# Kernel optimization log

Hardware: AMD Instinct MI355X
Metric: run time of the kernel (lower is better)

Reference implementation:

```python
import jax, jax.numpy as jnp
import numpy as np

V, J, NB = 6890, 52, 16
NPOSE = (J - 1) * 9  # 459 pose-blendshape features
# Standard SMPL-H kinematic tree: 22 body joints + left hand (wrist 20) + right hand (wrist 21)
PARENTS = np.array([
    -1, 0, 0, 0, 1, 2, 3, 4, 5, 6, 7, 8, 9, 9, 9, 12, 13, 14, 16, 17, 18, 19,
    20, 22, 23, 20, 25, 26, 20, 28, 29, 20, 31, 32, 20, 34, 35,
    21, 37, 38, 21, 40, 41, 21, 43, 44, 21, 46, 47, 21, 49, 50
], dtype=np.int32)


def rot6d_to_matrix(d6):
    # d6: (..., 6) -> (..., 3, 3), rows are the Gram-Schmidt basis (pytorch3d convention)
    a1, a2 = d6[..., :3], d6[..., 3:]
    b1 = a1 / jnp.linalg.norm(a1, axis=-1, keepdims=True)
    a2p = a2 - jnp.sum(b1 * a2, axis=-1, keepdims=True) * b1
    b2 = a2p / jnp.linalg.norm(a2p, axis=-1, keepdims=True)
    b3 = jnp.cross(b1, b2)
    return jnp.stack([b1, b2, b3], axis=-2)


def rigid_transform(rot_mats, joints):
    # rot_mats: (B, J, 3, 3); joints: (B, J, 3) -> relative transforms (B, J, 4, 4)
    rel = jnp.concatenate(
        [joints[..., :1, :], joints[..., 1:, :] - joints[..., PARENTS[1:], :]], axis=-2)
    tm = jnp.concatenate([rot_mats, rel[..., None]], axis=-1)  # (B, J, 3, 4)
    bottom = jnp.zeros(tm.shape[:-2] + (1, 4), dtype=tm.dtype).at[..., 0, 3].set(1.0)
    tm = jnp.concatenate([tm, bottom], axis=-2)  # (B, J, 4, 4)
    chain = [tm[..., 0, :, :]]
    for i in range(1, J):  # fixed 52-joint tree, unrolled
        chain.append(chain[int(PARENTS[i])] @ tm[..., i, :, :])
    transforms = jnp.stack(chain, axis=-3)  # (B, J, 4, 4)
    t_corr = jnp.einsum('bjcd,bjd->bjc', transforms[..., :3, :3], joints)
    return transforms.at[..., :3, 3].add(-t_corr)


def lbs_forward(body_pose, betas, global_orient, transl,
                v_template, shapedirs, posedirs, J_template, J_shapedirs, lbs_weights):
    full_pose = jnp.concatenate([global_orient, body_pose], axis=-2)  # (B, 52, 6)
    rot_mats = rot6d_to_matrix(full_pose)                              # (B, 52, 3, 3)
    joints = J_template + jnp.einsum('bk,jck->bjc', betas, J_shapedirs)
    A = rigid_transform(rot_mats, joints)                              # (B, 52, 4, 4)
    eye = jnp.eye(3, dtype=rot_mats.dtype)
    pose_feature = (rot_mats[..., 1:, :, :] - eye).reshape(rot_mats.shape[0], NPOSE)
    v_posed = (v_template
               + jnp.einsum('bk,vck->bvc', betas, shapedirs)
               + jnp.einsum('bk,kvc->bvc', pose_feature, posedirs))    # (B, V, 3)
    T = jnp.einsum('vj,bjcd->bvcd', lbs_weights, A)                    # (B, V, 4, 4)
    verts = jnp.einsum('bvcd,bvd->bvc', T[..., :3, :3], v_posed) + T[..., :3, 3]
    return verts + transl[..., None, :]


def setup_inputs() -> dict:
    key = jax.random.key(0)
    ks = jax.random.split(key, 10)
    B = 1024
    return {
        'body_pose': jax.random.normal(ks[0], (B, J - 1, 6), jnp.float32),
        'betas': jax.random.normal(ks[1], (B, NB), jnp.float32),
        'global_orient': jax.random.normal(ks[2], (B, 1, 6), jnp.float32),
        'transl': jax.random.normal(ks[3], (B, 3), jnp.float32),
        'v_template': jax.random.normal(ks[4], (V, 3), jnp.float32) * 0.3,
        'shapedirs': jax.random.normal(ks[5], (V, 3, NB), jnp.float32) * 0.01,
        'posedirs': jax.random.normal(ks[6], (NPOSE, V, 3), jnp.float32) * 0.01,
        'J_template': jax.random.normal(ks[7], (J, 3), jnp.float32) * 0.3,
        'J_shapedirs': jax.random.normal(ks[8], (J, 3, NB), jnp.float32) * 0.01,
        'lbs_weights': jax.nn.softmax(jax.random.normal(ks[9], (V, J), jnp.float32) * 2.0, axis=-1),
    }


def reference(body_pose, betas, global_orient, transl,
              v_template, shapedirs, posedirs, J_template, J_shapedirs, lbs_weights):
    return lbs_forward(body_pose, betas, global_orient, transl,
                       v_template, shapedirs, posedirs, J_template, J_shapedirs, lbs_weights)
```

## Files before the change

kernel.cpp:

```cpp
#include <hip/hip_runtime.h>

typedef unsigned short u16;
typedef __bf16  bf16x8 __attribute__((ext_vector_type(8)));
typedef float   f32x4  __attribute__((ext_vector_type(4)));
typedef unsigned int u32x4 __attribute__((ext_vector_type(4)));

#define B_SZ   1024
#define V_SZ   6890
#define VPADB  6912
#define J_SZ   52
#define NB_SZ  16
#define NPOSE  459
#define N3     20670
#define NPAD   20736
#define KG     480
#define KA     160
#define MROWS  12288

#define NK1    (B_SZ / 4)
#define NK0W   (VPADB / 64)
#define NK0    (648 * 15)

__constant__ int PARENTS_D[52] = {-1,0,0,0,1,2,3,4,5,6,7,8,9,9,9,12,13,14,16,17,18,19,20,22,23,
                                  20,25,26,20,28,29,20,31,32,20,34,35,21,37,38,21,40,41,21,43,44,
                                  21,46,47,21,49,50};

__device__ __forceinline__ u16 f2b(float f) {
  union { float f; unsigned u; } v; v.f = f;
  unsigned r = (v.u + 0x7FFFu + ((v.u >> 16) & 1u)) >> 16;
  return (u16)r;
}
__device__ __forceinline__ float b2f(u16 h) {
  union { unsigned u; float f; } v; v.u = ((unsigned)h) << 16;
  return v.f;
}
__device__ __forceinline__ void async16(const void* g, void* l) {
  __builtin_amdgcn_global_load_lds((const __attribute__((address_space(1))) void*)g,
                                   (__attribute__((address_space(3))) void*)l, 16, 0, 0);
}

__global__ __launch_bounds__(256) void k_prep(const float* __restrict__ posedirs,
                                              const float* __restrict__ shapedirs,
                                              const float* __restrict__ lbsw,
                                              const float* __restrict__ body_pose,
                                              const float* __restrict__ betas,
                                              const float* __restrict__ global_orient,
                                              const float* __restrict__ J_template,
                                              const float* __restrict__ J_shapedirs,
                                              u16* __restrict__ PDt,
                                              u16* __restrict__ WB,
                                              u16* __restrict__ AH,
                                              u16* __restrict__ PF)
{
  __shared__ __align__(16) char smem[35328];
  const int bid = blockIdx.x;
  const int tid = threadIdx.x;

  if (bid < NK1) {
    const int g = tid >> 6;
    const int t = tid & 63;
    const int b = bid * 4 + g;
    char* base = smem + g * 8832;
    float (*R)[9]   = (float(*)[9])(base);
    float (*jts)[3] = (float(*)[3])(base + 1872);
    float (*G)[12]  = (float(*)[12])(base + 2496);
    u16*   AHs      = (u16*)(base + 4992);

    for (int i = t; i < 12 * KA / 2; i += 64) ((unsigned*)AHs)[i] = 0u;

    if (t < J_SZ) {
      const float* d6 = (t == 0) ? &global_orient[(size_t)b * 6]
                                 : &body_pose[((size_t)b * 51 + (t - 1)) * 6];
      float a1x = d6[0], a1y = d6[1], a1z = d6[2];
      float a2x = d6[3], a2y = d6[4], a2z = d6[5];
      float inv1 = rsqrtf(a1x*a1x + a1y*a1y + a1z*a1z);
      float b1x = a1x*inv1, b1y = a1y*inv1, b1z = a1z*inv1;
      float d   = b1x*a2x + b1y*a2y + b1z*a2z;
      float ux = a2x - d*b1x, uy = a2y - d*b1y, uz = a2z - d*b1z;
      float inv2 = rsqrtf(ux*ux + uy*uy + uz*uz);
      float b2x = ux*inv2, b2y = uy*inv2, b2z = uz*inv2;
      float b3x = b1y*b2z - b1z*b2y;
      float b3y = b1z*b2x - b1x*b2z;
      float b3z = b1x*b2y - b1y*b2x;
      R[t][0]=b1x; R[t][1]=b1y; R[t][2]=b1z;
      R[t][3]=b2x; R[t][4]=b2y; R[t][5]=b2z;
      R[t][6]=b3x; R[t][7]=b3y; R[t][8]=b3z;
#pragma unroll
      for (int c = 0; c < 3; ++c) {
        float s = J_template[t*3 + c];
#pragma unroll
        for (int k = 0; k < NB_SZ; ++k)
          s += betas[(size_t)b*NB_SZ + k] * J_shapedirs[(t*3 + c)*NB_SZ + k];
        jts[t][c] = s;
      }
    }
    __syncthreads();

    if (t < 3) {
      const int c = t;
      G[0][c*4+0] = R[0][c*3+0];
      G[0][c*4+1] = R[0][c*3+1];
      G[0][c*4+2] = R[0][c*3+2];
      G[0][c*4+3] = jts[0][c];
      for (int j = 1; j < J_SZ; ++j) {
        int p = PARENTS_D[j];
        float r0 = jts[j][0] - jts[p][0];
        float r1 = jts[j][1] - jts[p][1];
        float r2 = jts[j][2] - jts[p][2];
        float g0 = G[p][c*4+0], g1 = G[p][c*4+1], g2 = G[p][c*4+2];
        G[j][c*4+0] = g0*R[j][0] + g1*R[j][3] + g2*R[j][6];
        G[j][c*4+1] = g0*R[j][1] + g1*R[j][4] + g2*R[j][7];
        G[j][c*4+2] = g0*R[j][2] + g1*R[j][5] + g2*R[j][8];
        G[j][c*4+3] = g0*r0 + g1*r1 + g2*r2 + G[p][c*4+3];
      }
    }
    __syncthreads();

    if (t < J_SZ) {
      float o[12];
#pragma unroll
      for (int i = 0; i < 12; ++i) o[i] = G[t][i];
#pragma unroll
      for (int c = 0; c < 3; ++c)
        o[c*4+3] -= o[c*4+0]*jts[t][0] + o[c*4+1]*jts[t][1] + o[c*4+2]*jts[t][2];
#pragma unroll
      for (int cd = 0; cd < 12; ++cd) {
        u16 hi = f2b(o[cd]);
        u16 lo = f2b(o[cd] - b2f(hi));
        AHs[cd*KA + t]        = hi;
        AHs[cd*KA + 52 + t]   = lo;
        AHs[cd*KA + 104 + t]  = hi;
      }
    }

    for (int k = t; k < KG; k += 64) {
      float val = 0.f;
      if (k < NPOSE) {
        int j  = k / 9 + 1;
        int rc = k - (j - 1) * 9;
        val = R[j][rc] - ((rc == 0 || rc == 4 || rc == 8) ? 1.f : 0.f);
      } else if (k < NPOSE + NB_SZ) {
        val = betas[(size_t)b*NB_SZ + (k - NPOSE)];
      }
      PF[(size_t)b*KG + k] = f2b(val);
    }

    __syncthreads();
    unsigned* dst = (unsigned*)(AH + (size_t)b * 12 * KA);
    for (int i = t; i < 12 * KA / 2; i += 64) dst[i] = ((const unsigned*)AHs)[i];

  } else if (bid < NK1 + NK0W) {
    u16* wtile = (u16*)smem;
    const int v0  = (bid - NK1) * 64;
    const int vl  = tid >> 2;
    const int v   = v0 + vl;
    const int jseg = (tid & 3) * 13;

    wtile[vl * KA + 156 + (tid & 3)] = 0;

#pragma unroll
    for (int jj = 0; jj < 13; ++jj) {
      int j = jseg + jj;
      float wv = (v < V_SZ) ? lbsw[(size_t)v * J_SZ + j] : 0.f;
      u16 hi = f2b(wv);
      u16 lo = f2b(wv - b2f(hi));
      wtile[vl * KA + j]        = hi;
      wtile[vl * KA + 52 + j]   = hi;
      wtile[vl * KA + 104 + j]  = lo;
    }
    __syncthreads();
    u32x4*       dst = (u32x4*)(WB + (size_t)v0 * KA);
    const u32x4* src = (const u32x4*)wtile;
    for (int i = tid; i < 64 * KA / 8; i += 256) dst[i] = src[i];

  } else {
    u16 (*tile)[33] = (u16(*)[33])smem;
    const int cb = bid - NK1 - NK0W;
    const int tx = tid & 31;
    const int ty = tid >> 5;
    const int n0 = (cb % 648) * 32;
    const int k0 = (cb / 648) * 32;
#pragma unroll
    for (int i = 0; i < 4; ++i) {
      int k = k0 + ty + i*8;
      int n = n0 + tx;
      float val = 0.f;
      if (n < N3) {
        if (k < NPOSE)              val = posedirs[(size_t)k * N3 + n];
        else if (k < NPOSE + NB_SZ) val = shapedirs[(size_t)n * NB_SZ + (k - NPOSE)];
      }
      tile[ty + i*8][tx] = f2b(val);
    }
    __syncthreads();
#pragma unroll
    for (int i = 0; i < 4; ++i) {
      int n = n0 + ty + i*8;
      int k = k0 + tx;
      int vv = n / 3;
      int cc = n - vv * 3;
      PDt[((size_t)cc * VPADB + vv) * KG + k] = tile[tx][ty + i*8];
    }
  }
}

__global__ __launch_bounds__(256) void k2_gemm(const u16* __restrict__ PF,
                                               const u16* __restrict__ PDt,
                                               const float* __restrict__ vtmpl,
                                               u16* __restrict__ VP)
{
  __shared__ __align__(16) u16 lA[2][4096];
  __shared__ __align__(16) u16 lB[2][4096];
  const int tid  = threadIdx.x;
  const int lane = tid & 63;
  const int w    = tid >> 6;
  const int n0   = blockIdx.x * 128;
  const int b0   = blockIdx.y * 128;
  const int moff = (w & 1) * 64;
  const int noff = (w >> 1) * 64;
  const int q    = lane >> 4;
  const int lrow = lane & 15;

  f32x4 acc[4][4];
#pragma unroll
  for (int i = 0; i < 4; ++i)
#pragma unroll
    for (int j = 0; j < 4; ++j) { f32x4 z = {0.f,0.f,0.f,0.f}; acc[i][j] = z; }

  int aoff[4], boff[4];
#pragma unroll
  for (int i = 0; i < 4; ++i) {
    int ra = moff + i*16 + lrow;
    aoff[i] = ra*32 + (q ^ ((ra + (ra >> 2)) & 3)) * 8;
    int rb = noff + i*16 + lrow;
    boff[i] = rb*32 + (q ^ ((rb + (rb >> 2)) & 3)) * 8;
  }
  int srow[2], schunk[2];
#pragma unroll
  for (int t = 0; t < 2; ++t) {
    int i = (t*4 + w)*64 + lane;
    int r = i >> 2;
    srow[t]   = r;
    schunk[t] = (i & 3) ^ ((r + (r >> 2)) & 3);
  }

#define K2_STAGE(buf, seg)                                                          \
  {                                                                                 \
    const int kk = (seg) * 32;                                                      \
    _Pragma("unroll")                                                               \
    for (int t = 0; t < 2; ++t) {                                                   \
      async16(PF  + (size_t)(b0 + srow[t])*KG + kk + schunk[t]*8,                   \
              &lA[buf][(t*4 + w)*512]);                                             \
      async16(PDt + (size_t)(n0 + srow[t])*KG + kk + schunk[t]*8,                   \
              &lB[buf][(t*4 + w)*512]);                                             \
    }                                                                               \
  }

  K2_STAGE(0, 0);

  for (int seg = 0; seg < 15; ++seg) {
    const int cur = seg & 1;
    if (seg < 14) K2_STAGE(cur ^ 1, seg + 1);
    __builtin_amdgcn_sched_barrier(0);
    if (seg < 14) asm volatile("s_waitcnt vmcnt(4)" ::: "memory");
    else          asm volatile("s_waitcnt vmcnt(0)" ::: "memory");
    __builtin_amdgcn_s_barrier();
    __builtin_amdgcn_sched_barrier(0);
    bf16x8 af[4], bfv[4];
#pragma unroll
    for (int i = 0; i < 4; ++i) af[i]  = *(const bf16x8*)&lA[cur][aoff[i]];
#pragma unroll
    for (int i = 0; i < 4; ++i) bfv[i] = *(const bf16x8*)&lB[cur][boff[i]];
#pragma unroll
    for (int i = 0; i < 4; ++i)
#pragma unroll
      for (int j = 0; j < 4; ++j)
        acc[i][j] = __builtin_amdgcn_mfma_f32_16x16x32_bf16(af[i], bfv[j], acc[i][j], 0, 0, 0);
    if (seg < 14) {
      __builtin_amdgcn_sched_barrier(0);
      __builtin_amdgcn_s_barrier();
    }
  }
#undef K2_STAGE

#pragma unroll
  for (int i = 0; i < 4; ++i) {
    int brow = b0 + moff + i*16 + q*4;
#pragma unroll
    for (int j = 0; j < 4; ++j) {
      int np = n0 + noff + j*16 + lrow;
      int vv = np % VPADB;
      int cc = np / VPADB;
      float bias = (vv < V_SZ) ? vtmpl[vv*3 + cc] : 0.f;
#pragma unroll
      for (int r = 0; r < 4; ++r)
        VP[(size_t)(brow + r)*NPAD + np] = f2b(acc[i][j][r] + bias);
    }
  }
}

__global__ __launch_bounds__(256) void k4_blend(const u16* __restrict__ AH,
                                                const u16* __restrict__ WB,
                                                const u16* __restrict__ VP,
                                                const float* __restrict__ transl,
                                                float* __restrict__ out)
{
  __shared__ __align__(16) u16 lA[2][4096];
  __shared__ __align__(16) u16 lB[2][4096];
  const int tid  = threadIdx.x;
  const int lane = tid & 63;
  const int w    = tid >> 6;
  const int n0   = blockIdx.x * 128;
  const int m0   = blockIdx.y * 128;
  const int moff = (w & 1) * 64;
  const int noff = (w >> 1) * 64;
  const int q    = lane >> 4;
  const int lrow = lane & 15;

  int srow[2], schunk[2];
#pragma unroll
  for (int t = 0; t < 2; ++t) {
    int i = (t*4 + w)*64 + lane;
    int r = i >> 2;
    srow[t]   = r;
    schunk[t] = (i & 3) ^ ((r + (r >> 2)) & 3);
  }

#define K4_STAGE(buf, seg)                                                          \
  {                                                                                 \
    const int kk = (seg) * 32;                                                      \
    _Pragma("unroll")                                                               \
    for (int t = 0; t < 2; ++t) {                                                   \
      async16(AH + (size_t)(m0 + srow[t])*KA + kk + schunk[t]*8,                    \
              &lA[buf][(t*4 + w)*512]);                                             \
      async16(WB + (size_t)(n0 + srow[t])*KA + kk + schunk[t]*8,                    \
              &lB[buf][(t*4 + w)*512]);                                             \
    }                                                                               \
  }

  int   bp[4], cp[4];
#pragma unroll
  for (int i = 0; i < 4; ++i) {
    int gq = (m0 + moff + i*16) / 4 + q;
    bp[i] = gq / 3;
    cp[i] = gq - bp[i]*3;
  }
  u16 pv[4][4][3];
#pragma unroll
  for (int i = 0; i < 4; ++i) {
    const u16* vpb = VP + (size_t)bp[i] * NPAD;
#pragma unroll
    for (int j = 0; j < 4; ++j) {
      const int v = n0 + noff + j*16 + lrow;
      pv[i][j][0] = vpb[0*VPADB + v];
      pv[i][j][1] = vpb[1*VPADB + v];
      pv[i][j][2] = vpb[2*VPADB + v];
    }
  }
  float tr[4];
#pragma unroll
  for (int i = 0; i < 4; ++i) tr[i] = transl[bp[i]*3 + cp[i]];

  K4_STAGE(0, 0);

  f32x4 acc[4][4];
#pragma unroll
  for (int i = 0; i < 4; ++i)
#pragma unroll
    for (int j = 0; j < 4; ++j) { f32x4 z = {0.f,0.f,0.f,0.f}; acc[i][j] = z; }

  int aoff[4], boff[4];
#pragma unroll
  for (int i = 0; i < 4; ++i) {
    int ra = moff + i*16 + lrow;
    aoff[i] = ra*32 + (q ^ ((ra + (ra >> 2)) & 3)) * 8;
    int rb = noff + i*16 + lrow;
    boff[i] = rb*32 + (q ^ ((rb + (rb >> 2)) & 3)) * 8;
  }

#pragma unroll
  for (int seg = 0; seg < 5; ++seg) {
    const int cur = seg & 1;
    if (seg < 4) K4_STAGE(cur ^ 1, seg + 1);
    __builtin_amdgcn_sched_barrier(0);
    if (seg < 4) asm volatile("s_waitcnt vmcnt(4)" ::: "memory");
    else         asm volatile("s_waitcnt vmcnt(0)" ::: "memory");
    __builtin_amdgcn_s_barrier();
    __builtin_amdgcn_sched_barrier(0);
    bf16x8 af[4], bfv[4];
#pragma unroll
    for (int i = 0; i < 4; ++i) af[i]  = *(const bf16x8*)&lA[cur][aoff[i]];
#pragma unroll
    for (int i = 0; i < 4; ++i) bfv[i] = *(const bf16x8*)&lB[cur][boff[i]];
#pragma unroll
    for (int i = 0; i < 4; ++i)
#pragma unroll
      for (int j = 0; j < 4; ++j)
        acc[i][j] = __builtin_amdgcn_mfma_f32_16x16x32_bf16(af[i], bfv[j], acc[i][j], 0, 0, 0);
    if (seg < 4) {
      __builtin_amdgcn_sched_barrier(0);
      __builtin_amdgcn_s_barrier();
    }
  }
#undef K4_STAGE

#pragma unroll
  for (int i = 0; i < 4; ++i) {
    float* ob = out + (size_t)bp[i] * (V_SZ * 3);
#pragma unroll
    for (int j = 0; j < 4; ++j) {
      const int v = n0 + noff + j*16 + lrow;
      if (v < V_SZ) {
        float p0 = b2f(pv[i][j][0]);
        float p1 = b2f(pv[i][j][1]);
        float p2 = b2f(pv[i][j][2]);
        f32x4 a = acc[i][j];
        ob[(size_t)v*3 + cp[i]] = a[0]*p0 + a[1]*p1 + a[2]*p2 + a[3] + tr[i];
      }
    }
  }
}

extern "C" void kernel_launch(void* const* d_in, const int* in_sizes, int n_in,
                              void* d_out, int out_size, void* d_ws, size_t ws_size,
                              hipStream_t stream) {
  const float* body_pose     = (const float*)d_in[0];
  const float* betas         = (const float*)d_in[1];
  const float* global_orient = (const float*)d_in[2];
  const float* transl        = (const float*)d_in[3];
  const float* v_template    = (const float*)d_in[4];
  const float* shapedirs     = (const float*)d_in[5];
  const float* posedirs      = (const float*)d_in[6];
  const float* J_template    = (const float*)d_in[7];
  const float* J_shapedirs   = (const float*)d_in[8];
  const float* lbsw          = (const float*)d_in[9];
  float* out = (float*)d_out;

  char* ws = (char*)d_ws;
  u16* PF  = (u16*)(ws);
  u16* AH  = (u16*)(ws + 1048576u);
  u16* WB  = (u16*)(ws + 6291456u);
  u16* PDt = (u16*)(ws + 8503296u);
  u16* VP  = (u16*)(ws + 28409856u);

  k_prep<<<dim3(NK1 + NK0W + NK0), dim3(256), 0, stream>>>(
      posedirs, shapedirs, lbsw, body_pose, betas, global_orient,
      J_template, J_shapedirs, PDt, WB, AH, PF);
  k2_gemm<<<dim3(162, 8), dim3(256), 0, stream>>>(PF, PDt, v_template, VP);
  k4_blend<<<dim3(VPADB / 128, MROWS / 128), dim3(256), 0, stream>>>(AH, WB, VP, transl, out);
}
```

Measured before the change: 253.0 us.

## Load GEMM operands directly to registers and remap blocks XCD-aware in both GEMMs

Both MFMA GEMM kernels stop staging A/B tiles through LDS with async global-to-LDS copies and barriers. Each wave now loads its bf16x8 fragments straight from global memory into double-buffered registers. The grids are also flattened to 1D, with a block-index remap that groups neighbouring tiles onto the same XCD for L2 reuse. This removes LDS traffic and barrier syncs, but every wave now fetches its own rows directly, so global and L2 load traffic grows and the loads are less coalesced.

```diff
diff --git a/kernel.cpp b/kernel.cpp
--- a/kernel.cpp
+++ b/kernel.cpp
@@ -33,10 +33,6 @@
 __device__ __forceinline__ float b2f(u16 h) {
   union { unsigned u; float f; } v; v.u = ((unsigned)h) << 16;
   return v.f;
-}
-__device__ __forceinline__ void async16(const void* g, void* l) {
-  __builtin_amdgcn_global_load_lds((const __attribute__((address_space(1))) void*)g,
-                                   (__attribute__((address_space(3))) void*)l, 16, 0, 0);
 }
 
 __global__ __launch_bounds__(256) void k_prep(const float* __restrict__ posedirs,
@@ -208,79 +204,46 @@
                                                const float* __restrict__ vtmpl,
                                                u16* __restrict__ VP)
 {
-  __shared__ __align__(16) u16 lA[2][4096];
-  __shared__ __align__(16) u16 lB[2][4096];
   const int tid  = threadIdx.x;
   const int lane = tid & 63;
   const int w    = tid >> 6;
-  const int n0   = blockIdx.x * 128;
-  const int b0   = blockIdx.y * 128;
+  const int W    = (blockIdx.x & 7) * 162 + (blockIdx.x >> 3);
+  const int n0   = (W >> 3) * 128;
+  const int b0   = (W & 7) * 128;
   const int moff = (w & 1) * 64;
   const int noff = (w >> 1) * 64;
   const int q    = lane >> 4;
   const int lrow = lane & 15;
 
+  const u16* Ab = PF  + (size_t)(b0 + moff + lrow) * KG + q * 8;
+  const u16* Bb = PDt + (size_t)(n0 + noff + lrow) * KG + q * 8;
+
   f32x4 acc[4][4];
 #pragma unroll
   for (int i = 0; i < 4; ++i)
 #pragma unroll
     for (int j = 0; j < 4; ++j) { f32x4 z = {0.f,0.f,0.f,0.f}; acc[i][j] = z; }
 
-  int aoff[4], boff[4];
-#pragma unroll
-  for (int i = 0; i < 4; ++i) {
-    int ra = moff + i*16 + lrow;
-    aoff[i] = ra*32 + (q ^ ((ra + (ra >> 2)) & 3)) * 8;
-    int rb = noff + i*16 + lrow;
-    boff[i] = rb*32 + (q ^ ((rb + (rb >> 2)) & 3)) * 8;
-  }
-  int srow[2], schunk[2];
-#pragma unroll
-  for (int t = 0; t < 2; ++t) {
-    int i = (t*4 + w)*64 + lane;
-    int r = i >> 2;
-    srow[t]   = r;
-    schunk[t] = (i & 3) ^ ((r + (r >> 2)) & 3);
-  }
-
-#define K2_STAGE(buf, seg)                                                          \
-  {                                                                                 \
-    const int kk = (seg) * 32;                                                      \
-    _Pragma("unroll")                                                               \
-    for (int t = 0; t < 2; ++t) {                                                   \
-      async16(PF  + (size_t)(b0 + srow[t])*KG + kk + schunk[t]*8,                   \
-              &lA[buf][(t*4 + w)*512]);                                             \
-      async16(PDt + (size_t)(n0 + srow[t])*KG + kk + schunk[t]*8,                   \
-              &lB[buf][(t*4 + w)*512]);                                             \
-    }                                                                               \
-  }
-
-  K2_STAGE(0, 0);
-
+  bf16x8 a[2][4], bfr[2][4];
+#define K2_LD(buf, seg)                                                        \
+  { _Pragma("unroll")                                                          \
+    for (int i = 0; i < 4; ++i) {                                              \
+      a[buf][i]   = *(const bf16x8*)(Ab + (size_t)i*16*KG + (seg)*32);         \
+      bfr[buf][i] = *(const bf16x8*)(Bb + (size_t)i*16*KG + (seg)*32);         \
+    } }
+
+  K2_LD(0, 0);
+#pragma unroll
   for (int seg = 0; seg < 15; ++seg) {
-    const int cur = seg & 1;
-    if (seg < 14) K2_STAGE(cur ^ 1, seg + 1);
-    __builtin_amdgcn_sched_barrier(0);
-    if (seg < 14) asm volatile("s_waitcnt vmcnt(4)" ::: "memory");
-    else          asm volatile("s_waitcnt vmcnt(0)" ::: "memory");
-    __builtin_amdgcn_s_barrier();
-    __builtin_amdgcn_sched_barrier(0);
-    bf16x8 af[4], bfv[4];
-#pragma unroll
-    for (int i = 0; i < 4; ++i) af[i]  = *(const bf16x8*)&lA[cur][aoff[i]];
-#pragma unroll
-    for (int i = 0; i < 4; ++i) bfv[i] = *(const bf16x8*)&lB[cur][boff[i]];
+    if (seg < 14) K2_LD((seg + 1) & 1, seg + 1);
+    const int c = seg & 1;
 #pragma unroll
     for (int i = 0; i < 4; ++i)
 #pragma unroll
       for (int j = 0; j < 4; ++j)
-        acc[i][j] = __builtin_amdgcn_mfma_f32_16x16x32_bf16(af[i], bfv[j], acc[i][j], 0, 0, 0);
-    if (seg < 14) {
-      __builtin_amdgcn_sched_barrier(0);
-      __builtin_amdgcn_s_barrier();
-    }
-  }
-#undef K2_STAGE
+        acc[i][j] = __builtin_amdgcn_mfma_f32_16x16x32_bf16(a[c][i], bfr[c][j], acc[i][j], 0, 0, 0);
+  }
+#undef K2_LD
 
 #pragma unroll
   for (int i = 0; i < 4; ++i) {
@@ -304,38 +267,46 @@
                                                 const float* __restrict__ transl,
                                                 float* __restrict__ out)
 {
-  __shared__ __align__(16) u16 lA[2][4096];
-  __shared__ __align__(16) u16 lB[2][4096];
   const int tid  = threadIdx.x;
   const int lane = tid & 63;
   const int w    = tid >> 6;
-  const int n0   = blockIdx.x * 128;
-  const int m0   = blockIdx.y * 128;
+  const int W    = (blockIdx.x & 7) * 648 + (blockIdx.x >> 3);
+  const int n0   = (W % 54) * 128;
+  const int m0   = (W / 54) * 128;
   const int moff = (w & 1) * 64;
   const int noff = (w >> 1) * 64;
   const int q    = lane >> 4;
   const int lrow = lane & 15;
 
-  int srow[2], schunk[2];
-#pragma unroll
-  for (int t = 0; t < 2; ++t) {
-    int i = (t*4 + w)*64 + lane;
-    int r = i >> 2;
-    srow[t]   = r;
-    schunk[t] = (i & 3) ^ ((r + (r >> 2)) & 3);
-  }
-
-#define K4_STAGE(buf, seg)                                                          \
-  {                                                                                 \
-    const int kk = (seg) * 32;                                                      \
-    _Pragma("unroll")                                                               \
-    for (int t = 0; t < 2; ++t) {                                                   \
-      async16(AH + (size_t)(m0 + srow[t])*KA + kk + schunk[t]*8,                    \
-              &lA[buf][(t*4 + w)*512]);                                             \
-      async16(WB + (size_t)(n0 + srow[t])*KA + kk + schunk[t]*8,                    \
-              &lB[buf][(t*4 + w)*512]);                                             \
-    }                                                                               \
-  }
+  const u16* Ab = AH + (size_t)(m0 + moff + lrow) * KA + q * 8;
+  const u16* Bb = WB + (size_t)(n0 + noff + lrow) * KA + q * 8;
+
+  f32x4 acc[4][4];
+#pragma unroll
+  for (int i = 0; i < 4; ++i)
+#pragma unroll
+    for (int j = 0; j < 4; ++j) { f32x4 z = {0.f,0.f,0.f,0.f}; acc[i][j] = z; }
+
+  bf16x8 a[2][4], bfr[2][4];
+#define K4_LD(buf, seg)                                                        \
+  { _Pragma("unroll")                                                          \
+    for (int i = 0; i < 4; ++i) {                                              \
+      a[buf][i]   = *(const bf16x8*)(Ab + (size_t)i*16*KA + (seg)*32);         \
+      bfr[buf][i] = *(const bf16x8*)(Bb + (size_t)i*16*KA + (seg)*32);         \
+    } }
+
+  K4_LD(0, 0);
+#pragma unroll
+  for (int seg = 0; seg < 5; ++seg) {
+    if (seg < 4) K4_LD((seg + 1) & 1, seg + 1);
+    const int c = seg & 1;
+#pragma unroll
+    for (int i = 0; i < 4; ++i)
+#pragma unroll
+      for (int j = 0; j < 4; ++j)
+        acc[i][j] = __builtin_amdgcn_mfma_f32_16x16x32_bf16(a[c][i], bfr[c][j], acc[i][j], 0, 0, 0);
+  }
+#undef K4_LD
 
   int   bp[4], cp[4];
 #pragma unroll
@@ -359,49 +330,6 @@
   float tr[4];
 #pragma unroll
   for (int i = 0; i < 4; ++i) tr[i] = transl[bp[i]*3 + cp[i]];
-
-  K4_STAGE(0, 0);
-
-  f32x4 acc[4][4];
-#pragma unroll
-  for (int i = 0; i < 4; ++i)
-#pragma unroll
-    for (int j = 0; j < 4; ++j) { f32x4 z = {0.f,0.f,0.f,0.f}; acc[i][j] = z; }
-
-  int aoff[4], boff[4];
-#pragma unroll
-  for (int i = 0; i < 4; ++i) {
-    int ra = moff + i*16 + lrow;
-    aoff[i] = ra*32 + (q ^ ((ra + (ra >> 2)) & 3)) * 8;
-    int rb = noff + i*16 + lrow;
-    boff[i] = rb*32 + (q ^ ((rb + (rb >> 2)) & 3)) * 8;
-  }
-
-#pragma unroll
-  for (int seg = 0; seg < 5; ++seg) {
-    const int cur = seg & 1;
-    if (seg < 4) K4_STAGE(cur ^ 1, seg + 1);
-    __builtin_amdgcn_sched_barrier(0);
-    if (seg < 4) asm volatile("s_waitcnt vmcnt(4)" ::: "memory");
-    else         asm volatile("s_waitcnt vmcnt(0)" ::: "memory");
-    __builtin_amdgcn_s_barrier();
-    __builtin_amdgcn_sched_barrier(0);
-    bf16x8 af[4], bfv[4];
-#pragma unroll
-    for (int i = 0; i < 4; ++i) af[i]  = *(const bf16x8*)&lA[cur][aoff[i]];
-#pragma unroll
-    for (int i = 0; i < 4; ++i) bfv[i] = *(const bf16x8*)&lB[cur][boff[i]];
-#pragma unroll
-    for (int i = 0; i < 4; ++i)
-#pragma unroll
-      for (int j = 0; j < 4; ++j)
-        acc[i][j] = __builtin_amdgcn_mfma_f32_16x16x32_bf16(af[i], bfv[j], acc[i][j], 0, 0, 0);
-    if (seg < 4) {
-      __builtin_amdgcn_sched_barrier(0);
-      __builtin_amdgcn_s_barrier();
-    }
-  }
-#undef K4_STAGE
 
 #pragma unroll
   for (int i = 0; i < 4; ++i) {
@@ -413,8 +341,8 @@
         float p0 = b2f(pv[i][j][0]);
         float p1 = b2f(pv[i][j][1]);
         float p2 = b2f(pv[i][j][2]);
-        f32x4 a = acc[i][j];
-        ob[(size_t)v*3 + cp[i]] = a[0]*p0 + a[1]*p1 + a[2]*p2 + a[3] + tr[i];
+        f32x4 aa = acc[i][j];
+        ob[(size_t)v*3 + cp[i]] = aa[0]*p0 + aa[1]*p1 + aa[2]*p2 + aa[3] + tr[i];
       }
     }
   }
@@ -445,6 +373,6 @@
   k_prep<<<dim3(NK1 + NK0W + NK0), dim3(256), 0, stream>>>(
       posedirs, shapedirs, lbsw, body_pose, betas, global_orient,
       J_template, J_shapedirs, PDt, WB, AH, PF);
-  k2_gemm<<<dim3(162, 8), dim3(256), 0, stream>>>(PF, PDt, v_template, VP);
-  k4_blend<<<dim3(VPADB / 128, MROWS / 128), dim3(256), 0, stream>>>(AH, WB, VP, transl, out);
-}
+  k2_gemm<<<dim3(162 * 8), dim3(256), 0, stream>>>(PF, PDt, v_template, VP);
+  k4_blend<<<dim3(54 * 96), dim3(256), 0, stream>>>(AH, WB, VP, transl, out);
+}
```

Result: slower. 282.4 us (+11.7%).
